# Kernel tuning notes

Measured on AMD Instinct MI355X. Metric: run time of the kernel, lower is better.

Reference implementation:

```python
import jax, jax.numpy as jnp
import numpy as np


def setup_inputs() -> dict:
    key = jax.random.key(0)
    ks = jax.random.split(key, 8)
    B, C, N = 4, 64, 32768
    d = C // 8
    inp = {
        "x": jax.random.normal(ks[0], (B, C, N), dtype=jnp.float32),
        "Wq": jax.random.normal(ks[1], (d, C), dtype=jnp.float32) * 0.1,
        "bq": jax.random.normal(ks[2], (d,), dtype=jnp.float32) * 0.1,
        "Wk": jax.random.normal(ks[3], (d, C), dtype=jnp.float32) * 0.1,
        "bk": jax.random.normal(ks[4], (d,), dtype=jnp.float32) * 0.1,
        "Wv": jax.random.normal(ks[5], (C, C), dtype=jnp.float32) * 0.1,
        "bv": jax.random.normal(ks[6], (C,), dtype=jnp.float32) * 0.1,
        # nn.Parameter(torch.zeros(1)) in the original; nonzero here so the
        # attention branch actually contributes to the output.
        "gamma": jax.random.normal(ks[7], (1,), dtype=jnp.float32) * 0.1,
        "window_size": 512,
        "stride": 256,
        "pooling_factor": 2,
    }
    return inp


def reference(x, Wq, bq, Wk, bk, Wv, bv, gamma, window_size, stride, pooling_factor):
    B, C, N = x.shape
    # conv1x1 projections are pointwise -> apply once on the full signal
    q = jnp.einsum("dc,bcn->bdn", Wq, x) + bq[None, :, None]  # [B, d, N]
    k = jnp.einsum("dc,bcn->bdn", Wk, x) + bk[None, :, None]  # [B, d, N]
    v = jnp.einsum("ec,bcn->ben", Wv, x) + bv[None, :, None]  # [B, C, N]

    starts = jnp.arange(0, N - window_size + 1, stride)              # [W]
    idx = starts[:, None] + jnp.arange(window_size)[None, :]         # [W, ws]

    qw = q[:, :, idx]  # [B, d, W, ws]
    kw = k[:, :, idx]
    vw = v[:, :, idx]  # [B, C, W, ws]
    xw = x[:, :, idx]

    energy = jnp.einsum("bdwi,bdwj->bwij", qw, kw)                   # [B, W, ws, ws]
    attn = jax.nn.softmax(energy, axis=-1)
    # torch: bmm(v, attn^T) -> out[c,i] = sum_j v[c,j] * attn[i,j]
    out_local = jnp.einsum("bcwj,bwij->bcwi", vw, attn)              # [B, C, W, ws]

    contrib = gamma[0] * out_local + xw
    out = jnp.zeros_like(x).at[:, :, idx].add(contrib)               # overlap-add
    counts = jnp.zeros((N,), x.dtype).at[idx].add(1.0)               # overlap count
    out = out / counts[None, None, :]

    P = pooling_factor
    Np = (N // P) * P
    out = out[:, :, :Np].reshape(B, C, N // P, P).max(axis=-1)       # MaxPool1d(P)
    return out
```

## Files before the change

kernel.cpp:

```cpp
#include <hip/hip_runtime.h>
#include <hip/hip_bf16.h>

#define BB 4
#define CC 64
#define DD 8
#define NN 32768
#define WW 512
#define STR 256
#define NWIN 127
#define LOG2E 1.4426950408889634f

typedef short bf16x8 __attribute__((ext_vector_type(8)));
typedef float f32x4 __attribute__((ext_vector_type(4)));
typedef float f32x16 __attribute__((ext_vector_type(16)));

__device__ __forceinline__ unsigned int pack_bf16(float lo, float hi) {
    __hip_bfloat162 h = __float22bfloat162_rn(make_float2(lo, hi));
    unsigned int r; __builtin_memcpy(&r, &h, 4);
    return r;
}
__device__ __forceinline__ unsigned short to_bf16(float f) {
    __hip_bfloat16 h = __float2bfloat16(f);
    unsigned short r; __builtin_memcpy(&r, &h, 2);
    return r;
}
__device__ __forceinline__ float bf2f(unsigned short s) {
    union { unsigned int u; float f; } v; v.u = ((unsigned int)s) << 16;
    return v.f;
}
__device__ __forceinline__ float fast_exp2(float x) {
#if __has_builtin(__builtin_amdgcn_exp2f)
    return __builtin_amdgcn_exp2f(x);
#else
    float r; asm("v_exp_f32 %0, %1" : "=v"(r) : "v"(x)); return r;
#endif
}
__device__ __forceinline__ void plswap(unsigned int &x, unsigned int &y) {
    asm("v_permlane32_swap_b32 %0, %1" : "+v"(x), "+v"(y));
}
__device__ __forceinline__ bf16x8 pack8(float a0, float a1, float a2, float a3,
                                        float a4, float a5, float a6, float a7) {
    union { bf16x8 v; unsigned int u[4]; } r;
    r.u[0] = pack_bf16(a0, a1); r.u[1] = pack_bf16(a2, a3);
    r.u[2] = pack_bf16(a4, a5); r.u[3] = pack_bf16(a6, a7);
    return r.v;
}
__device__ __forceinline__ bf16x8 words4(unsigned int w0, unsigned int w1,
                                         unsigned int w2, unsigned int w3) {
    union { bf16x8 v; unsigned int u[4]; } r;
    r.u[0] = w0; r.u[1] = w1; r.u[2] = w2; r.u[3] = w3;
    return r.v;
}

__global__ __launch_bounds__(256) void qkv_kernel(
    const float* __restrict__ x,
    const float* __restrict__ Wq, const float* __restrict__ bq,
    const float* __restrict__ Wk, const float* __restrict__ bk,
    const float* __restrict__ Wv, const float* __restrict__ bv,
    unsigned short* __restrict__ qout, unsigned short* __restrict__ kout,
    unsigned short* __restrict__ vout)
{
    const int t = threadIdx.x;
    const int lane = t & 63, wv = t >> 6;
    const int a = lane & 15, g = lane >> 4;

    bf16x8 wf[5][2];
    #pragma unroll
    for (int T = 0; T < 5; ++T) {
        const float* wrow;
        float scale = 1.f;
        if (T == 0) {
            if (a < 8) { wrow = Wq + a*CC; scale = LOG2E; }
            else       { wrow = Wk + (a-8)*CC; }
        } else {
            wrow = Wv + ((T-1)*16 + a)*CC;
        }
        #pragma unroll
        for (int h = 0; h < 2; ++h) {
            float4 w0 = *(const float4*)(wrow + h*32 + g*8);
            float4 w1 = *(const float4*)(wrow + h*32 + g*8 + 4);
            wf[T][h] = pack8(w0.x*scale, w0.y*scale, w0.z*scale, w0.w*scale,
                             w1.x*scale, w1.y*scale, w1.z*scale, w1.w*scale);
        }
    }
    f32x4 bias[5];
    {
        const int r = g*4;
        #pragma unroll
        for (int u = 0; u < 4; ++u) {
            int rr = r + u;
            bias[0][u] = (rr < 8) ? bq[rr]*LOG2E : bk[rr-8];
        }
        #pragma unroll
        for (int T = 1; T < 5; ++T)
            #pragma unroll
            for (int u = 0; u < 4; ++u)
                bias[T][u] = bv[(T-1)*16 + r + u];
    }

    const int wave_id = blockIdx.x*4 + wv;
    #pragma unroll 1
    for (int it = 0; it < 2; ++it) {
        const int chunk = wave_id + it*4096;
        const int b = chunk >> 11;
        const int n0 = (chunk & 2047) * 16;
        const int n = n0 + a;
        const float* xcol = x + (size_t)b*CC*NN + n;

        float xv0[8], xv1[8];
        #pragma unroll
        for (int u = 0; u < 8; ++u) xv0[u] = xcol[(size_t)(g*8 + u)*NN];
        #pragma unroll
        for (int u = 0; u < 8; ++u) xv1[u] = xcol[(size_t)(32 + g*8 + u)*NN];
        bf16x8 xb0 = pack8(xv0[0],xv0[1],xv0[2],xv0[3],xv0[4],xv0[5],xv0[6],xv0[7]);
        bf16x8 xb1 = pack8(xv1[0],xv1[1],xv1[2],xv1[3],xv1[4],xv1[5],xv1[6],xv1[7]);

        f32x4 acc[5];
        #pragma unroll
        for (int T = 0; T < 5; ++T) {
            acc[T] = __builtin_amdgcn_mfma_f32_16x16x32_bf16(wf[T][0], xb0, bias[T], 0, 0, 0);
            acc[T] = __builtin_amdgcn_mfma_f32_16x16x32_bf16(wf[T][1], xb1, acc[T], 0, 0, 0);
        }

        {
            unsigned int lo = pack_bf16(acc[0][0], acc[0][1]);
            unsigned int hi = pack_bf16(acc[0][2], acc[0][3]);
            unsigned short* base = ((g < 2) ? qout : kout) + ((size_t)b*NN + n)*8 + (g & 1)*4;
            *(int2*)base = make_int2((int)lo, (int)hi);
        }
        #pragma unroll
        for (int T = 1; T < 5; ++T) {
            #pragma unroll
            for (int u = 0; u < 4; ++u) {
                const int e = (T-1)*16 + g*4 + u;
                vout[((size_t)b*CC + e)*NN + n] = to_bf16(acc[T][u]);
            }
        }
    }
}

__global__ __launch_bounds__(256) void attn_kernel(
    const unsigned short* __restrict__ qg, const unsigned short* __restrict__ kg,
    const unsigned short* __restrict__ vg,
    unsigned short* __restrict__ accE, unsigned short* __restrict__ accO)
{
    __shared__ unsigned short sK[WW][8];
    __shared__ unsigned short sV[2][64][36];
    __shared__ float sInv[4][32];
    const int t = threadIdx.x;
    const int lane = t & 63, wv = t >> 6;
    const int l31 = lane & 31, hi = lane >> 5;
    int bid = (blockIdx.x & 7)*254 + (blockIdx.x >> 3);
    const int q2 = bid & 3; bid >>= 2;
    const int w = bid % NWIN, b = bid / NWIN;
    const int nwin = STR * w;
    const int i0 = q2*128 + wv*32;

    const unsigned short* qbase = qg + ((size_t)b*NN + nwin + i0)*8;
    const unsigned short* kbase = kg + ((size_t)b*NN + nwin)*8;
    const unsigned short* vsrc  = vg + ((size_t)b*CC + (t >> 2))*NN + nwin + (t & 3)*8;

    #pragma unroll
    for (int m = 0; m < 2; ++m) {
        const int row = m*256 + t;
        *(int4*)&sK[row][0] = *(const int4*)(kbase + (size_t)row*8);
    }
    {
        int4 r = *(const int4*)vsrc;
        unsigned short* dst = &sV[0][t >> 2][(t & 3)*8];
        *(int2*)dst = *(int2*)&r;
        *(int2*)(dst + 4) = *((int2*)&r + 1);
    }

    const bf16x8 zf = {};
    bf16x8 qf;
    {
        bf16x8 raw = *(const bf16x8*)(qbase + (size_t)l31*8);
        qf = hi ? zf : raw;
    }

    f32x16 acc[2] = {};
    float2 rsum2 = make_float2(0.f, 0.f);

    __syncthreads();

    f32x16 Ecur;
    {
        const f32x16 z16 = {};
        bf16x8 kc = *(const bf16x8*)&sK[l31][0];
        Ecur = __builtin_amdgcn_mfma_f32_32x32x16_bf16(kc, qf, z16, 0, 0, 0);
    }

    for (int jt = 0; jt < 16; ++jt) {
        const int j0 = jt*32;
        const int cur = jt & 1;
        int4 stg;
        if (jt < 15) stg = *(const int4*)(vsrc + j0 + 32);
        f32x16 Enext;
        if (jt < 15) {
            const f32x16 z16 = {};
            bf16x8 kn = *(const bf16x8*)&sK[j0 + 32 + l31][0];
            Enext = __builtin_amdgcn_mfma_f32_32x32x16_bf16(kn, qf, z16, 0, 0, 0);
        }
        bf16x8 vf[2][2];
        #pragma unroll
        for (int ct = 0; ct < 2; ++ct)
            #pragma unroll
            for (int sl = 0; sl < 2; ++sl) {
                const unsigned short* p = &sV[cur][ct*32 + l31][sl*16 + hi*8];
                union { bf16x8 v; int2 d[2]; } u;
                u.d[0] = *(const int2*)p;
                u.d[1] = *(const int2*)(p + 4);
                vf[ct][sl] = u.v;
            }
        float p[16];
        #pragma unroll
        for (int r = 0; r < 16; ++r) p[r] = fast_exp2(Ecur[r]);
        float2 s0 = make_float2(p[0],  p[1])  + make_float2(p[2],  p[3]);
        float2 s1 = make_float2(p[4],  p[5])  + make_float2(p[6],  p[7]);
        float2 s2 = make_float2(p[8],  p[9])  + make_float2(p[10], p[11]);
        float2 s3 = make_float2(p[12], p[13]) + make_float2(p[14], p[15]);
        rsum2 += (s0 + s1) + (s2 + s3);
        unsigned int wd[8];
        #pragma unroll
        for (int tw = 0; tw < 8; ++tw) wd[tw] = pack_bf16(p[2*tw], p[2*tw+1]);
        unsigned int F0 = wd[0], F2 = wd[2]; plswap(F0, F2);
        unsigned int F1 = wd[1], F3 = wd[3]; plswap(F1, F3);
        unsigned int G0 = wd[4], G2 = wd[6]; plswap(G0, G2);
        unsigned int G1 = wd[5], G3 = wd[7]; plswap(G1, G3);
        bf16x8 pa0 = words4(F0, F1, F2, F3);
        bf16x8 pa1 = words4(G0, G1, G2, G3);
        #pragma unroll
        for (int ct = 0; ct < 2; ++ct) {
            acc[ct] = __builtin_amdgcn_mfma_f32_32x32x16_bf16(pa0, vf[ct][0], acc[ct], 0, 0, 0);
            acc[ct] = __builtin_amdgcn_mfma_f32_32x32x16_bf16(pa1, vf[ct][1], acc[ct], 0, 0, 0);
        }
        if (jt < 15) {
            unsigned short* dst = &sV[cur ^ 1][t >> 2][(t & 3)*8];
            *(int2*)dst = *(int2*)&stg;
            *(int2*)(dst + 4) = *((int2*)&stg + 1);
        }
        __syncthreads();
        Ecur = Enext;
    }

    float r = rsum2.x + rsum2.y;
    r += __shfl_xor(r, 32);
    if (lane < 32) sInv[wv][lane] = 1.f / r;
    f32x4 invv[4];
    #pragma unroll
    for (int g = 0; g < 4; ++g)
        invv[g] = *(const f32x4*)&sInv[wv][8*g + 4*hi];

    unsigned short* ob = ((w & 1) ? accO : accE) + (size_t)b*CC*NN + nwin + i0;
    #pragma unroll
    for (int ct = 0; ct < 2; ++ct) {
        unsigned short* cbase = ob + (size_t)(ct*32 + l31)*NN;
        #pragma unroll
        for (int g = 0; g < 4; ++g) {
            float a0 = acc[ct][4*g+0] * invv[g][0];
            float a1 = acc[ct][4*g+1] * invv[g][1];
            float a2 = acc[ct][4*g+2] * invv[g][2];
            float a3 = acc[ct][4*g+3] * invv[g][3];
            int2 pw = make_int2((int)pack_bf16(a0, a1), (int)pack_bf16(a2, a3));
            *(int2*)(cbase + 8*g + 4*hi) = pw;
        }
    }
}

__global__ __launch_bounds__(256) void final_kernel(
    const float* __restrict__ x,
    const unsigned short* __restrict__ accE, const unsigned short* __restrict__ accO,
    const float* __restrict__ gamma, float* __restrict__ out)
{
    const size_t tid = (size_t)blockIdx.x*256 + threadIdx.x;
    const size_t base = tid*8;
    const int n = (int)(base & (NN-1));
    const float g = gamma[0];

    float xv[8];
    *(float4*)&xv[0] = *(const float4*)&x[base];
    *(float4*)&xv[4] = *(const float4*)&x[base+4];
    int4 aeq = *(const int4*)&accE[base];
    const unsigned int* ae = (const unsigned int*)&aeq;

    float s[8];
    if (n >= STR && n < NN - STR) {
        int4 aoq = *(const int4*)&accO[base];
        const unsigned int* ao = (const unsigned int*)&aoq;
        #pragma unroll
        for (int u = 0; u < 4; ++u) {
            float e0 = bf2f((unsigned short)(ae[u] & 0xffff));
            float e1 = bf2f((unsigned short)(ae[u] >> 16));
            float o0 = bf2f((unsigned short)(ao[u] & 0xffff));
            float o1 = bf2f((unsigned short)(ao[u] >> 16));
            s[2*u]   = fmaf(g, (e0 + o0)*0.5f, xv[2*u]);
            s[2*u+1] = fmaf(g, (e1 + o1)*0.5f, xv[2*u+1]);
        }
    } else {
        #pragma unroll
        for (int u = 0; u < 4; ++u) {
            float e0 = bf2f((unsigned short)(ae[u] & 0xffff));
            float e1 = bf2f((unsigned short)(ae[u] >> 16));
            s[2*u]   = fmaf(g, e0, xv[2*u]);
            s[2*u+1] = fmaf(g, e1, xv[2*u+1]);
        }
    }
    float4 o = make_float4(fmaxf(s[0], s[1]), fmaxf(s[2], s[3]),
                           fmaxf(s[4], s[5]), fmaxf(s[6], s[7]));
    *(float4*)&out[tid*4] = o;
}

extern "C" void kernel_launch(void* const* d_in, const int* in_sizes, int n_in,
                              void* d_out, int out_size, void* d_ws, size_t ws_size,
                              hipStream_t stream)
{
    const float* x    = (const float*)d_in[0];
    const float* Wq   = (const float*)d_in[1];
    const float* bq   = (const float*)d_in[2];
    const float* Wk   = (const float*)d_in[3];
    const float* bk   = (const float*)d_in[4];
    const float* Wv   = (const float*)d_in[5];
    const float* bv   = (const float*)d_in[6];
    const float* gamma= (const float*)d_in[7];

    unsigned short* q    = (unsigned short*)d_ws;
    unsigned short* k    = q + (size_t)BB*NN*DD;
    unsigned short* v    = k + (size_t)BB*NN*DD;
    unsigned short* accE = v + (size_t)BB*CC*NN;
    unsigned short* accO = accE + (size_t)BB*CC*NN;
    float* out = (float*)d_out;

    qkv_kernel<<<1024, 256, 0, stream>>>(x, Wq, bq, Wk, bk, Wv, bv, q, k, v);
    attn_kernel<<<BB*NWIN*4, 256, 0, stream>>>(q, k, v, accE, accO);
    final_kernel<<<BB*CC*NN/8/256, 256, 0, stream>>>(x, accE, accO, gamma, out);
}
```

Before: 73.44 us.

## Tile V and attention accumulators for direct register loads, drop LDS staging

```diff
diff --git a/kernel.cpp b/kernel.cpp
--- a/kernel.cpp
+++ b/kernel.cpp
@@ -51,6 +51,7 @@
     r.u[0] = w0; r.u[1] = w1; r.u[2] = w2; r.u[3] = w3;
     return r.v;
 }
+
 
 __global__ __launch_bounds__(256) void qkv_kernel(
     const float* __restrict__ x,
@@ -128,12 +129,13 @@
             unsigned short* base = ((g < 2) ? qout : kout) + ((size_t)b*NN + n)*8 + (g & 1)*4;
             *(int2*)base = make_int2((int)lo, (int)hi);
         }
+        unsigned short* vtb = vout + (((size_t)b*1024 + (n>>5))*4 + ((n>>3)&3))*512 + (n&7);
         #pragma unroll
         for (int T = 1; T < 5; ++T) {
             #pragma unroll
             for (int u = 0; u < 4; ++u) {
                 const int e = (T-1)*16 + g*4 + u;
-                vout[((size_t)b*CC + e)*NN + n] = to_bf16(acc[T][u]);
+                vtb[e*8] = to_bf16(acc[T][u]);
             }
         }
     }
@@ -144,8 +146,6 @@
     const unsigned short* __restrict__ vg,
     unsigned short* __restrict__ accE, unsigned short* __restrict__ accO)
 {
-    __shared__ unsigned short sK[WW][8];
-    __shared__ unsigned short sV[2][64][36];
     __shared__ float sInv[4][32];
     const int t = threadIdx.x;
     const int lane = t & 63, wv = t >> 6;
@@ -158,19 +158,7 @@
 
     const unsigned short* qbase = qg + ((size_t)b*NN + nwin + i0)*8;
     const unsigned short* kbase = kg + ((size_t)b*NN + nwin)*8;
-    const unsigned short* vsrc  = vg + ((size_t)b*CC + (t >> 2))*NN + nwin + (t & 3)*8;
-
-    #pragma unroll
-    for (int m = 0; m < 2; ++m) {
-        const int row = m*256 + t;
-        *(int4*)&sK[row][0] = *(const int4*)(kbase + (size_t)row*8);
-    }
-    {
-        int4 r = *(const int4*)vsrc;
-        unsigned short* dst = &sV[0][t >> 2][(t & 3)*8];
-        *(int2*)dst = *(int2*)&r;
-        *(int2*)(dst + 4) = *((int2*)&r + 1);
-    }
+    const unsigned short* vt = vg + (((size_t)b*1024 + 8*w)*4 + 2*hi)*512 + (size_t)l31*8;
 
     const bf16x8 zf = {};
     bf16x8 qf;
@@ -182,40 +170,32 @@
     f32x16 acc[2] = {};
     float2 rsum2 = make_float2(0.f, 0.f);
 
-    __syncthreads();
-
-    f32x16 Ecur;
-    {
+    bf16x8 kc = *(const bf16x8*)(kbase + (size_t)l31*8);
+    bf16x8 vc[2][2];
+    #pragma unroll
+    for (int ct = 0; ct < 2; ++ct)
+        #pragma unroll
+        for (int sl = 0; sl < 2; ++sl)
+            vc[ct][sl] = *(const bf16x8*)(vt + (size_t)(sl*2)*512 + ct*256);
+
+    #pragma unroll 2
+    for (int jt = 0; jt < 16; ++jt) {
+        bf16x8 kn = kc;
+        bf16x8 vn[2][2] = {{vc[0][0], vc[0][1]}, {vc[1][0], vc[1][1]}};
+        if (jt < 15) {
+            kn = *(const bf16x8*)(kbase + (size_t)(jt*32 + 32 + l31)*8);
+            #pragma unroll
+            for (int ct = 0; ct < 2; ++ct)
+                #pragma unroll
+                for (int sl = 0; sl < 2; ++sl)
+                    vn[ct][sl] = *(const bf16x8*)(vt + (size_t)((jt+1)*4 + sl*2)*512 + ct*256);
+        }
+
         const f32x16 z16 = {};
-        bf16x8 kc = *(const bf16x8*)&sK[l31][0];
-        Ecur = __builtin_amdgcn_mfma_f32_32x32x16_bf16(kc, qf, z16, 0, 0, 0);
-    }
-
-    for (int jt = 0; jt < 16; ++jt) {
-        const int j0 = jt*32;
-        const int cur = jt & 1;
-        int4 stg;
-        if (jt < 15) stg = *(const int4*)(vsrc + j0 + 32);
-        f32x16 Enext;
-        if (jt < 15) {
-            const f32x16 z16 = {};
-            bf16x8 kn = *(const bf16x8*)&sK[j0 + 32 + l31][0];
-            Enext = __builtin_amdgcn_mfma_f32_32x32x16_bf16(kn, qf, z16, 0, 0, 0);
-        }
-        bf16x8 vf[2][2];
-        #pragma unroll
-        for (int ct = 0; ct < 2; ++ct)
-            #pragma unroll
-            for (int sl = 0; sl < 2; ++sl) {
-                const unsigned short* p = &sV[cur][ct*32 + l31][sl*16 + hi*8];
-                union { bf16x8 v; int2 d[2]; } u;
-                u.d[0] = *(const int2*)p;
-                u.d[1] = *(const int2*)(p + 4);
-                vf[ct][sl] = u.v;
-            }
+        f32x16 E = __builtin_amdgcn_mfma_f32_32x32x16_bf16(kc, qf, z16, 0, 0, 0);
         float p[16];
         #pragma unroll
-        for (int r = 0; r < 16; ++r) p[r] = fast_exp2(Ecur[r]);
+        for (int r = 0; r < 16; ++r) p[r] = fast_exp2(E[r]);
         float2 s0 = make_float2(p[0],  p[1])  + make_float2(p[2],  p[3]);
         float2 s1 = make_float2(p[4],  p[5])  + make_float2(p[6],  p[7]);
         float2 s2 = make_float2(p[8],  p[9])  + make_float2(p[10], p[11]);
@@ -232,16 +212,15 @@
         bf16x8 pa1 = words4(G0, G1, G2, G3);
         #pragma unroll
         for (int ct = 0; ct < 2; ++ct) {
-            acc[ct] = __builtin_amdgcn_mfma_f32_32x32x16_bf16(pa0, vf[ct][0], acc[ct], 0, 0, 0);
-            acc[ct] = __builtin_amdgcn_mfma_f32_32x32x16_bf16(pa1, vf[ct][1], acc[ct], 0, 0, 0);
-        }
-        if (jt < 15) {
-            unsigned short* dst = &sV[cur ^ 1][t >> 2][(t & 3)*8];
-            *(int2*)dst = *(int2*)&stg;
-            *(int2*)(dst + 4) = *((int2*)&stg + 1);
-        }
-        __syncthreads();
-        Ecur = Enext;
+            acc[ct] = __builtin_amdgcn_mfma_f32_32x32x16_bf16(pa0, vc[ct][0], acc[ct], 0, 0, 0);
+            acc[ct] = __builtin_amdgcn_mfma_f32_32x32x16_bf16(pa1, vc[ct][1], acc[ct], 0, 0, 0);
+        }
+        kc = kn;
+        #pragma unroll
+        for (int ct = 0; ct < 2; ++ct)
+            #pragma unroll
+            for (int sl = 0; sl < 2; ++sl)
+                vc[ct][sl] = vn[ct][sl];
     }
 
     float r = rsum2.x + rsum2.y;
@@ -252,10 +231,11 @@
     for (int g = 0; g < 4; ++g)
         invv[g] = *(const f32x4*)&sInv[wv][8*g + 4*hi];
 
-    unsigned short* ob = ((w & 1) ? accO : accE) + (size_t)b*CC*NN + nwin + i0;
+    unsigned short* ob = ((w & 1) ? accO : accE)
+        + ((size_t)b*1024 + ((nwin + i0) >> 5))*4*512 + 4*hi;
     #pragma unroll
     for (int ct = 0; ct < 2; ++ct) {
-        unsigned short* cbase = ob + (size_t)(ct*32 + l31)*NN;
+        unsigned short* cbase = ob + (ct*32 + l31)*8;
         #pragma unroll
         for (int g = 0; g < 4; ++g) {
             float a0 = acc[ct][4*g+0] * invv[g][0];
@@ -263,7 +243,7 @@
             float a2 = acc[ct][4*g+2] * invv[g][2];
             float a3 = acc[ct][4*g+3] * invv[g][3];
             int2 pw = make_int2((int)pack_bf16(a0, a1), (int)pack_bf16(a2, a3));
-            *(int2*)(cbase + 8*g + 4*hi) = pw;
+            *(int2*)(cbase + (size_t)g*512) = pw;
         }
     }
 }
@@ -276,17 +256,20 @@
     const size_t tid = (size_t)blockIdx.x*256 + threadIdx.x;
     const size_t base = tid*8;
     const int n = (int)(base & (NN-1));
+    const int c = (int)((base >> 15) & (CC-1));
+    const int b = (int)(base >> 21);
     const float g = gamma[0];
+    const size_t tadr = (((size_t)b*1024 + (n >> 5))*4 + ((n >> 3) & 3))*512 + c*8;
 
     float xv[8];
     *(float4*)&xv[0] = *(const float4*)&x[base];
     *(float4*)&xv[4] = *(const float4*)&x[base+4];
-    int4 aeq = *(const int4*)&accE[base];
+    int4 aeq = *(const int4*)&accE[tadr];
     const unsigned int* ae = (const unsigned int*)&aeq;
 
     float s[8];
     if (n >= STR && n < NN - STR) {
-        int4 aoq = *(const int4*)&accO[base];
+        int4 aoq = *(const int4*)&accO[tadr];
         const unsigned int* ao = (const unsigned int*)&aoq;
         #pragma unroll
         for (int u = 0; u < 4; ++u) {
```

After: 77.52 us. 5.6% more time.
